# Optimization experiments

Hardware: AMD Instinct MI355X
Metric: run time of the kernel (lower is better)

The kernel has to match this reference:

```python
import jax, jax.numpy as jnp
import numpy as np

_J6 = jnp.array([[0,0,0,0,0,1],[0,0,0,0,-1,0],[0,0,0,1,0,0],[0,0,1,0,0,0],[0,-1,0,0,0,0],[1,0,0,0,0,0]], dtype=jnp.float32)
# pairs (i,j) from combinations(range(4),2)
_PI = jnp.array([0,0,0,1,1,2])
_PJ = jnp.array([1,2,3,2,3,3])

def exterior(p1, p2):
    # p1, p2: [B,T,H,4] -> Plucker line coords [B,T,H,6], L2-normalized
    L = p1[..., _PI] * p2[..., _PJ] - p1[..., _PJ] * p2[..., _PI]
    n = jnp.clip(jnp.linalg.norm(L, axis=-1, keepdims=True), 1e-12)
    return L / n

def setup_inputs() -> dict:
    key = jax.random.key(0)
    ks = jax.random.split(key, 8)
    B, T, D, H = 2, 2048, 1024, 16
    pd = 4
    s = 0.02
    return {
        "x": jax.random.normal(ks[0], (B, T, D), jnp.float32),
        "w_qkv": jax.random.normal(ks[1], (3 * D, D), jnp.float32) * s,
        "b_qkv": jnp.zeros((3 * D,), jnp.float32),
        "w1_write": jax.random.normal(ks[2], (pd * H, D), jnp.float32) * s,
        "w2_write": jax.random.normal(ks[3], (pd * H, D), jnp.float32) * s,
        "w1_read": jax.random.normal(ks[4], (pd * H, D), jnp.float32) * s,
        "w2_read": jax.random.normal(ks[5], (pd * H, D), jnp.float32) * s,
        "w_out": jax.random.normal(ks[6], (D, D), jnp.float32) * s,
        "b_out": jnp.zeros((D,), jnp.float32),
        "decay_logits": jnp.full((H,), 4.6, jnp.float32),
        "bias_scale": jnp.full((H,), 0.1, jnp.float32),
    }

def reference(x, w_qkv, b_qkv, w1_write, w2_write, w1_read, w2_read, w_out, b_out, decay_logits, bias_scale):
    B, T, D = x.shape
    H = decay_logits.shape[0]
    dh = D // H
    pd = w1_write.shape[0] // H
    scale = dh ** -0.5

    qkv = (x @ w_qkv.T + b_qkv).reshape(B, T, 3, H, dh)
    qkv = jnp.transpose(qkv, (2, 0, 3, 1, 4))  # [3,B,H,T,dh]
    q, k, v = qkv[0], qkv[1], qkv[2]
    std_logits = jnp.einsum('bhqd,bhkd->bhqk', q, k) * scale

    x_prev = jnp.concatenate([jnp.zeros((B, 1, D), x.dtype), x[:, :-1]], axis=1)
    w1 = (x_prev @ w1_write.T).reshape(B, T, H, pd)
    w2 = (x @ w2_write.T).reshape(B, T, H, pd)
    write_lines = exterior(w1, w2)  # [B,T,H,6]
    r1 = (x @ w1_read.T).reshape(B, T, H, pd)
    r2 = (x @ w2_read.T).reshape(B, T, H, pd)
    read_lines = exterior(r1, r2)

    J_write = jnp.einsum('bthi,ij->bthj', write_lines, _J6)
    incidence = jnp.einsum('bqhp,bkhp->bhqk', read_lines, J_write)  # [B,H,T,T]

    decays = jax.nn.sigmoid(decay_logits)  # [H]
    pos = jnp.arange(T, dtype=x.dtype)
    diffs = pos[:, None] - pos[None, :]  # [T,T], q - k
    past = diffs > 0
    diffs_pos = jnp.where(past, diffs, 0.0)
    weights = (decays[:, None, None] ** diffs_pos[None]) * past[None].astype(x.dtype)  # [H,T,T]

    bias = incidence * weights[None] * bias_scale[None, :, None, None]
    logits = std_logits + bias
    causal_mask = diffs < 0  # k > q -> masked
    logits = jnp.where(causal_mask[None, None], -jnp.inf, logits)
    attn = jax.nn.softmax(logits, axis=-1)
    out = jnp.einsum('bhqk,bhkd->bqhd', attn, v).reshape(B, T, D)
    return out @ w_out.T + b_out
```

## Files before the change

### kernel.cpp

```cpp
#include <hip/hip_runtime.h>
#include <hip/hip_bf16.h>

using bhalf = __hip_bfloat16;
typedef __bf16 bf16x8 __attribute__((ext_vector_type(8)));
typedef __bf16 bf16x2 __attribute__((ext_vector_type(2)));
typedef float f32x4 __attribute__((ext_vector_type(4)));

#define B_DIM 2
#define T_DIM 2048
#define D_DIM 1024
#define H_DIM 16
#define DH 64

struct bh8 { bhalf v[8]; };
struct bh4 { bhalf v[4]; };

__device__ __forceinline__ bf16x8 load_bf16x8(const bhalf* p) {
    return __builtin_bit_cast(bf16x8, *(const uint4*)p);
}
__device__ __forceinline__ bf16x8 zero_bf16x8() {
    uint4 z; z.x = 0; z.y = 0; z.z = 0; z.w = 0;
    return __builtin_bit_cast(bf16x8, z);
}
__device__ __forceinline__ void stage8_cvt(bhalf* dst, const float* src) {
    float4 a = *(const float4*)src;
    float4 b = *(const float4*)(src + 4);
    bh8 t;
    t.v[0] = __float2bfloat16(a.x); t.v[1] = __float2bfloat16(a.y);
    t.v[2] = __float2bfloat16(a.z); t.v[3] = __float2bfloat16(a.w);
    t.v[4] = __float2bfloat16(b.x); t.v[5] = __float2bfloat16(b.y);
    t.v[6] = __float2bfloat16(b.z); t.v[7] = __float2bfloat16(b.w);
    *(uint4*)dst = __builtin_bit_cast(uint4, t);
}

#define GLD16(gp, lp) __builtin_amdgcn_global_load_lds( \
    (const __attribute__((address_space(1))) void*)(gp), \
    (__attribute__((address_space(3))) void*)(lp), 16, 0, 0)

#define SX  4194304
#define SW  3145728
#define SL  65536
#define SO  1048576
__global__ __launch_bounds__(256) void cvt_all(
    const float* __restrict__ x, const float* __restrict__ wqkv,
    const float* __restrict__ w1w, const float* __restrict__ w2w,
    const float* __restrict__ w1r, const float* __restrict__ w2r,
    const float* __restrict__ wout,
    bhalf* __restrict__ xbf, bhalf* __restrict__ wcat, bhalf* __restrict__ woutbf)
{
    int i = (blockIdx.x * 256 + threadIdx.x) * 8;
    if (i < SX) { stage8_cvt(xbf + i, x + i); return; }
    i -= SX;
    if (i < SW) { stage8_cvt(wcat + i, wqkv + i); return; }
    i -= SW;
    if (i < SL) { stage8_cvt(wcat + SW + i, w1w + i); return; }
    i -= SL;
    if (i < SL) { stage8_cvt(wcat + SW + SL + i, w2w + i); return; }
    i -= SL;
    if (i < SL) { stage8_cvt(wcat + SW + 2 * SL + i, w1r + i); return; }
    i -= SL;
    if (i < SL) { stage8_cvt(wcat + SW + 3 * SL + i, w2r + i); return; }
    i -= SL;
    if (i < SO) { stage8_cvt(woutbf + i, wout + i); }
}

__device__ __forceinline__ void gemm128_mainloop(
    const bhalf* __restrict__ A, const bhalf* __restrict__ B, int K,
    bhalf* As, bhalf* Bs, f32x4 acc[4][4])
{
    const int tid = threadIdx.x;
    const int wave = tid >> 6, lane = tid & 63;
    const int ln = lane & 15, lg = lane >> 4;
    const int wr = (wave >> 1) * 64, wc = (wave & 1) * 64;
    const int lrow = lane >> 3;
    const int lcol = (lane & 7) * 8;

    for (int kt = 0; kt < K; kt += 64) {
        __syncthreads();
#pragma unroll
        for (int i = 0; i < 4; ++i) {
            int idx = __builtin_amdgcn_readfirstlane(wave * 4 + i);
            GLD16(A + (size_t)(idx * 8 + lrow) * K + kt + lcol, As + idx * 512);
            GLD16(B + (size_t)(idx * 8 + lrow) * K + kt + lcol, Bs + idx * 512);
        }
        __syncthreads();
#pragma unroll
        for (int ks = 0; ks < 2; ++ks) {
            bf16x8 af[4], bfr[4];
#pragma unroll
            for (int mt = 0; mt < 4; ++mt)
                af[mt] = load_bf16x8(As + (wr + mt * 16 + ln) * 64 + ks * 32 + lg * 8);
#pragma unroll
            for (int nt = 0; nt < 4; ++nt)
                bfr[nt] = load_bf16x8(Bs + (wc + nt * 16 + ln) * 64 + ks * 32 + lg * 8);
#pragma unroll
            for (int mt = 0; mt < 4; ++mt)
#pragma unroll
                for (int nt = 0; nt < 4; ++nt)
                    acc[mt][nt] = __builtin_amdgcn_mfma_f32_16x16x32_bf16(af[mt], bfr[nt], acc[mt][nt], 0, 0, 0);
        }
    }
}

__global__ __launch_bounds__(256) void qkv_lines_gemm128(
    const bhalf* __restrict__ x, const bhalf* __restrict__ wcat, const float* __restrict__ bqkv,
    bhalf* __restrict__ qo, bhalf* __restrict__ ko, bhalf* __restrict__ vt,
    float* __restrict__ proj)
{
    __shared__ bhalf As[128 * 64];
    __shared__ bhalf Bs[128 * 64];
    f32x4 acc[4][4] = {};
    gemm128_mainloop(x + (size_t)blockIdx.x * 128 * D_DIM,
                     wcat + (size_t)blockIdx.y * 128 * D_DIM, D_DIM, As, Bs, acc);
    const int wave = threadIdx.x >> 6, lane = threadIdx.x & 63;
    const int ln = lane & 15, lg = lane >> 4;
    const int wr = (wave >> 1) * 64, wc = (wave & 1) * 64;
    const int trip = (blockIdx.y * 128) >> 10;

    if (trip == 2) {
#pragma unroll
        for (int nt = 0; nt < 4; ++nt) {
            int n = blockIdx.y * 128 + wc + nt * 16 + ln;
            float bias = bqkv[n];
            int h = (n >> 6) & 15, d = n & 63;
#pragma unroll
            for (int mt = 0; mt < 4; ++mt) {
                int tok0 = blockIdx.x * 128 + wr + mt * 16 + lg * 4;
                int b = tok0 >> 11, t0 = tok0 & (T_DIM - 1);
                bh4 pk;
#pragma unroll
                for (int r = 0; r < 4; ++r)
                    pk.v[r] = __float2bfloat16(acc[mt][nt][r] + bias);
                *(uint2*)&vt[(((size_t)(b * H_DIM + h)) * DH + d) * T_DIM + t0] =
                    __builtin_bit_cast(uint2, pk);
            }
        }
    } else {
#pragma unroll
        for (int nt = 0; nt < 4; ++nt) {
            int n = blockIdx.y * 128 + wc + nt * 16 + ln;
            int h = (n >> 6) & 15, d = n & 63;
            float bias = (trip < 3) ? bqkv[n] : 0.f;
#pragma unroll
            for (int mt = 0; mt < 4; ++mt)
#pragma unroll
                for (int r = 0; r < 4; ++r) {
                    int tok = blockIdx.x * 128 + wr + mt * 16 + lg * 4 + r;
                    int b = tok >> 11, t = tok & (T_DIM - 1);
                    float y = acc[mt][nt][r] + bias;
                    if (trip == 0) {
                        qo[(((size_t)(b * H_DIM + h)) * T_DIM + t) * DH + d] = __float2bfloat16(y * 0.125f);
                    } else if (trip == 1) {
                        ko[(((size_t)(b * H_DIM + h)) * T_DIM + t) * DH + d] = __float2bfloat16(y);
                    } else {
                        proj[(size_t)tok * 256 + (n - 3072)] = y;
                    }
                }
        }
    }
}

__global__ __launch_bounds__(256) void out_gemm64(
    const bhalf* __restrict__ a, const bhalf* __restrict__ w, const float* __restrict__ bo,
    float* __restrict__ out)
{
    __shared__ bhalf As[64 * 64];
    __shared__ bhalf Bs[64 * 64];
    const int tid = threadIdx.x;
    const int wave = tid >> 6, lane = tid & 63;
    const int ln = lane & 15, lg = lane >> 4;
    const int lrow = lane >> 3;
    const int lcol = (lane & 7) * 8;
    const bhalf* A = a + (size_t)blockIdx.x * 64 * D_DIM;
    const bhalf* B = w + (size_t)blockIdx.y * 64 * D_DIM;
    f32x4 acc[4] = {};

    for (int kt = 0; kt < D_DIM; kt += 64) {
        __syncthreads();
#pragma unroll
        for (int i = 0; i < 2; ++i) {
            int idx = __builtin_amdgcn_readfirstlane(wave * 2 + i);
            GLD16(A + (size_t)(idx * 8 + lrow) * D_DIM + kt + lcol, As + idx * 512);
            GLD16(B + (size_t)(idx * 8 + lrow) * D_DIM + kt + lcol, Bs + idx * 512);
        }
        __syncthreads();
#pragma unroll
        for (int ks = 0; ks < 2; ++ks) {
            bf16x8 af = load_bf16x8(As + (wave * 16 + ln) * 64 + ks * 32 + lg * 8);
#pragma unroll
            for (int nt = 0; nt < 4; ++nt) {
                bf16x8 bfr = load_bf16x8(Bs + (nt * 16 + ln) * 64 + ks * 32 + lg * 8);
                acc[nt] = __builtin_amdgcn_mfma_f32_16x16x32_bf16(af, bfr, acc[nt], 0, 0, 0);
            }
        }
    }
#pragma unroll
    for (int nt = 0; nt < 4; ++nt) {
        int n = blockIdx.y * 64 + nt * 16 + ln;
        float bias = bo[n];
#pragma unroll
        for (int r = 0; r < 4; ++r) {
            int tok = blockIdx.x * 64 + wave * 16 + lg * 4 + r;
            out[(size_t)tok * D_DIM + n] = acc[nt][r] + bias;
        }
    }
}

__global__ __launch_bounds__(256) void build_lines(
    const float* __restrict__ proj, const float* __restrict__ bias_scale,
    const float* __restrict__ decay_logits,
    bhalf* __restrict__ read8, bhalf* __restrict__ jw8)
{
    int id = blockIdx.x * 256 + threadIdx.x;
    int tok = id >> 4, h = id & 15;
    int b = tok >> 11, t = tok & (T_DIM - 1);
    const float* pr = proj + (size_t)tok * 256;

    float p1[4], p2[4], r1[4], r2[4];
#pragma unroll
    for (int i = 0; i < 4; ++i) {
        p1[i] = (t > 0) ? pr[-256 + h * 4 + i] : 0.f;
        p2[i] = pr[64 + h * 4 + i];
        r1[i] = pr[128 + h * 4 + i];
        r2[i] = pr[192 + h * 4 + i];
    }
    float Lw[6], Lr[6];
    {
        Lw[0] = p1[0] * p2[1] - p1[1] * p2[0];
        Lw[1] = p1[0] * p2[2] - p1[2] * p2[0];
        Lw[2] = p1[0] * p2[3] - p1[3] * p2[0];
        Lw[3] = p1[1] * p2[2] - p1[2] * p2[1];
        Lw[4] = p1[1] * p2[3] - p1[3] * p2[1];
        Lw[5] = p1[2] * p2[3] - p1[3] * p2[2];
        float n2 = 0.f;
#pragma unroll
        for (int j = 0; j < 6; ++j) n2 += Lw[j] * Lw[j];
        float inv = 1.f / fmaxf(sqrtf(n2), 1e-12f);
#pragma unroll
        for (int j = 0; j < 6; ++j) Lw[j] *= inv;
    }
    {
        Lr[0] = r1[0] * r2[1] - r1[1] * r2[0];
        Lr[1] = r1[0] * r2[2] - r1[2] * r2[0];
        Lr[2] = r1[0] * r2[3] - r1[3] * r2[0];
        Lr[3] = r1[1] * r2[2] - r1[2] * r2[1];
        Lr[4] = r1[1] * r2[3] - r1[3] * r2[1];
        Lr[5] = r1[2] * r2[3] - r1[3] * r2[2];
        float n2 = 0.f;
#pragma unroll
        for (int j = 0; j < 6; ++j) n2 += Lr[j] * Lr[j];
        float inv = 1.f / fmaxf(sqrtf(n2), 1e-12f);
#pragma unroll
        for (int j = 0; j < 6; ++j) Lr[j] *= inv;
    }
    float decay = 1.f / (1.f + __expf(-decay_logits[h]));
    float l2d = log2f(decay);
    float bs = bias_scale[h] * exp2f(-(float)t * l2d);
    size_t base = (((size_t)(b * H_DIM + h)) * T_DIM + t) * 8;
    read8[base + 0] = __float2bfloat16(Lr[0]);
    read8[base + 1] = __float2bfloat16(Lr[1]);
    read8[base + 2] = __float2bfloat16(Lr[2]);
    read8[base + 3] = __float2bfloat16(Lr[3]);
    read8[base + 4] = __float2bfloat16(Lr[4]);
    read8[base + 5] = __float2bfloat16(Lr[5]);
    read8[base + 6] = __float2bfloat16(0.f);
    read8[base + 7] = __float2bfloat16(0.f);
    jw8[base + 0] = __float2bfloat16(Lw[5] * bs);
    jw8[base + 1] = __float2bfloat16(-Lw[4] * bs);
    jw8[base + 2] = __float2bfloat16(Lw[3] * bs);
    jw8[base + 3] = __float2bfloat16(Lw[2] * bs);
    jw8[base + 4] = __float2bfloat16(-Lw[1] * bs);
    jw8[base + 5] = __float2bfloat16(Lw[0] * bs);
    jw8[base + 6] = __float2bfloat16(0.f);
    jw8[base + 7] = __float2bfloat16(0.f);
}

template<bool DIAG>
__device__ __forceinline__ void tile_step(
    const f32x4& z0, const f32x4& z1, const f32x4& i0, const f32x4& i1,
    int rq, int kb, const float* aq, int lg, int ln, bhalf* pl, float* lp)
{
    const float LOG2E = 1.44269504f;
#pragma unroll
    for (int r = 0; r < 4; ++r) {
        float p0, p1;
        if (DIAG) {
            int diff0 = rq + lg * 4 + r - (kb + 2 * ln);
            float s0 = z0[r] + ((diff0 > 0) ? i0[r] * aq[r] : 0.f);
            p0 = (diff0 < 0) ? 0.f : exp2f(s0 * LOG2E);
            int diff1 = diff0 - 1;
            float s1 = z1[r] + ((diff1 > 0) ? i1[r] * aq[r] : 0.f);
            p1 = (diff1 < 0) ? 0.f : exp2f(s1 * LOG2E);
        } else {
            p0 = exp2f(fmaf(i0[r], aq[r], z0[r]) * LOG2E);
            p1 = exp2f(fmaf(i1[r], aq[r], z1[r]) * LOG2E);
        }
        bf16x2 h2;
        h2.x = (__bf16)p0;
        h2.y = (__bf16)p1;
        *(unsigned int*)&pl[(lg * 4 + r) * 40 + 2 * ln] = __builtin_bit_cast(unsigned int, h2);
        lp[r] += p0 + p1;
    }
}

__global__ __launch_bounds__(256) void attn_kernel(
    const bhalf* __restrict__ q, const bhalf* __restrict__ k, const bhalf* __restrict__ vt,
    const bhalf* __restrict__ read8, const bhalf* __restrict__ jw8,
    const float* __restrict__ decay_logits, bhalf* __restrict__ attn_out)
{
    __shared__ float sm[4352];
    const int wave = threadIdx.x >> 6, lane = threadIdx.x & 63;
    const int ln = lane & 15, lg = lane >> 4;
    const int bx = blockIdx.x;
    const int xcd = bx & 7;
    const int slot = bx >> 3;
    const int hbid = xcd * 4 + (slot >> 6);
    const int h = hbid & 15, b = hbid >> 4;
    const int qa = slot & 63;
    const int qb = 127 - qa;
    const int rqa = qa * 16, rqb = qb * 16;
    const size_t hb = (size_t)(b * H_DIM + h);
    const bhalf* qh = q + hb * T_DIM * DH;
    const bhalf* kh = k + hb * T_DIM * DH;
    const bhalf* vh = vt + hb * DH * T_DIM;
    const bhalf* r8 = read8 + hb * T_DIM * 8;
    const bhalf* j8 = jw8 + hb * T_DIM * 8;

    bhalf* plA = (bhalf*)sm + wave * 640;
    bhalf* plB = (bhalf*)sm + 2560 + wave * 640;

    bf16x8 zf = zero_bf16x8();
    bf16x8 qA0 = load_bf16x8(qh + (rqa + ln) * DH + lg * 8);
    bf16x8 qA1 = load_bf16x8(qh + (rqa + ln) * DH + 32 + lg * 8);
    bf16x8 qB0 = load_bf16x8(qh + (rqb + ln) * DH + lg * 8);
    bf16x8 qB1 = load_bf16x8(qh + (rqb + ln) * DH + 32 + lg * 8);
    bf16x8 rfA = (lane < 16) ? load_bf16x8(r8 + (size_t)(rqa + ln) * 8) : zf;
    bf16x8 rfB = (lane < 16) ? load_bf16x8(r8 + (size_t)(rqb + ln) * 8) : zf;

    float decay = 1.f / (1.f + __expf(-decay_logits[h]));
    float l2d = log2f(decay);
    float aqA[4], aqB[4];
#pragma unroll
    for (int r = 0; r < 4; ++r) {
        aqA[r] = exp2f((float)(rqa + lg * 4 + r) * l2d);
        aqB[r] = exp2f((float)(rqb + lg * 4 + r) * l2d);
    }

    f32x4 oA[4] = {}, oB[4] = {};
    float lpA[4] = {0.f, 0.f, 0.f, 0.f}, lpB[4] = {0.f, 0.f, 0.f, 0.f};

    const int nca = qa / 2 + 1, ncb = qb / 2 + 1;
    for (int c = wave; c < ncb; c += 4) {
        const int kb = c * 32;
        bf16x8 k00 = load_bf16x8(kh + (kb + 2 * ln) * DH + lg * 8);
        bf16x8 k01 = load_bf16x8(kh + (kb + 2 * ln) * DH + 32 + lg * 8);
        bf16x8 k10 = load_bf16x8(kh + (kb + 2 * ln + 1) * DH + lg * 8);
        bf16x8 k11 = load_bf16x8(kh + (kb + 2 * ln + 1) * DH + 32 + lg * 8);
        bf16x8 j0 = (lane < 16) ? load_bf16x8(j8 + (size_t)(kb + 2 * ln) * 8) : zf;
        bf16x8 j1 = (lane < 16) ? load_bf16x8(j8 + (size_t)(kb + 2 * ln + 1) * 8) : zf;
        bf16x8 vf0 = load_bf16x8(vh + (size_t)(ln) * T_DIM + kb + lg * 8);
        bf16x8 vf1 = load_bf16x8(vh + (size_t)(16 + ln) * T_DIM + kb + lg * 8);
        bf16x8 vf2 = load_bf16x8(vh + (size_t)(32 + ln) * T_DIM + kb + lg * 8);
        bf16x8 vf3 = load_bf16x8(vh + (size_t)(48 + ln) * T_DIM + kb + lg * 8);
        const bool doA = (c < nca);

        {
            f32x4 z0 = {}, z1 = {}, i0 = {}, i1 = {};
            z0 = __builtin_amdgcn_mfma_f32_16x16x32_bf16(qB0, k00, z0, 0, 0, 0);
            z0 = __builtin_amdgcn_mfma_f32_16x16x32_bf16(qB1, k01, z0, 0, 0, 0);
            i0 = __builtin_amdgcn_mfma_f32_16x16x32_bf16(rfB, j0, i0, 0, 0, 0);
            z1 = __builtin_amdgcn_mfma_f32_16x16x32_bf16(qB0, k10, z1, 0, 0, 0);
            z1 = __builtin_amdgcn_mfma_f32_16x16x32_bf16(qB1, k11, z1, 0, 0, 0);
            i1 = __builtin_amdgcn_mfma_f32_16x16x32_bf16(rfB, j1, i1, 0, 0, 0);
            if (c == ncb - 1) tile_step<true >(z0, z1, i0, i1, rqb, kb, aqB, lg, ln, plB, lpB);
            else              tile_step<false>(z0, z1, i0, i1, rqb, kb, aqB, lg, ln, plB, lpB);
        }
        if (doA) {
            f32x4 z0 = {}, z1 = {}, i0 = {}, i1 = {};
            z0 = __builtin_amdgcn_mfma_f32_16x16x32_bf16(qA0, k00, z0, 0, 0, 0);
            z0 = __builtin_amdgcn_mfma_f32_16x16x32_bf16(qA1, k01, z0, 0, 0, 0);
            i0 = __builtin_amdgcn_mfma_f32_16x16x32_bf16(rfA, j0, i0, 0, 0, 0);
            z1 = __builtin_amdgcn_mfma_f32_16x16x32_bf16(qA0, k10, z1, 0, 0, 0);
            z1 = __builtin_amdgcn_mfma_f32_16x16x32_bf16(qA1, k11, z1, 0, 0, 0);
            i1 = __builtin_amdgcn_mfma_f32_16x16x32_bf16(rfA, j1, i1, 0, 0, 0);
            if (c == nca - 1) tile_step<true >(z0, z1, i0, i1, rqa, kb, aqA, lg, ln, plA, lpA);
            else              tile_step<false>(z0, z1, i0, i1, rqa, kb, aqA, lg, ln, plA, lpA);
        }
        __asm__ volatile("s_waitcnt lgkmcnt(0)" ::: "memory");
        {
            bf16x8 pf = load_bf16x8(plB + ln * 40 + lg * 8);
            oB[0] = __builtin_amdgcn_mfma_f32_16x16x32_bf16(pf, vf0, oB[0], 0, 0, 0);
            oB[1] = __builtin_amdgcn_mfma_f32_16x16x32_bf16(pf, vf1, oB[1], 0, 0, 0);
            oB[2] = __builtin_amdgcn_mfma_f32_16x16x32_bf16(pf, vf2, oB[2], 0, 0, 0);
            oB[3] = __builtin_amdgcn_mfma_f32_16x16x32_bf16(pf, vf3, oB[3], 0, 0, 0);
        }
        if (doA) {
            bf16x8 pf = load_bf16x8(plA + ln * 40 + lg * 8);
            oA[0] = __builtin_amdgcn_mfma_f32_16x16x32_bf16(pf, vf0, oA[0], 0, 0, 0);
            oA[1] = __builtin_amdgcn_mfma_f32_16x16x32_bf16(pf, vf1, oA[1], 0, 0, 0);
            oA[2] = __builtin_amdgcn_mfma_f32_16x16x32_bf16(pf, vf2, oA[2], 0, 0, 0);
            oA[3] = __builtin_amdgcn_mfma_f32_16x16x32_bf16(pf, vf3, oA[3], 0, 0, 0);
        }
    }

#pragma unroll
    for (int r = 0; r < 4; ++r) {
#pragma unroll
        for (int off = 1; off < 16; off <<= 1) {
            lpA[r] += __shfl_xor(lpA[r], off, 16);
            lpB[r] += __shfl_xor(lpB[r], off, 16);
        }
    }

    const int row = threadIdx.x >> 4;
    const int c4 = (threadIdx.x & 15) * 4;

    __syncthreads();
#pragma unroll
    for (int r = 0; r < 4; ++r) {
        if (ln == 0) sm[wave * 1088 + (lg * 4 + r) * 68 + 64] = lpA[r];
#pragma unroll
        for (int nt = 0; nt < 4; ++nt)
            sm[wave * 1088 + (lg * 4 + r) * 68 + nt * 16 + ln] = oA[nt][r];
    }
    __syncthreads();
    {
        float l = 0.f;
#pragma unroll
        for (int w = 0; w < 4; ++w) l += sm[w * 1088 + row * 68 + 64];
        float4 acc = {0.f, 0.f, 0.f, 0.f};
#pragma unroll
        for (int w = 0; w < 4; ++w) {
            float4 t = *(const float4*)&sm[w * 1088 + row * 68 + c4];
            acc.x += t.x; acc.y += t.y; acc.z += t.z; acc.w += t.w;
        }
        float invl = 1.f / l;
        bh4 pk;
        pk.v[0] = __float2bfloat16(acc.x * invl);
        pk.v[1] = __float2bfloat16(acc.y * invl);
        pk.v[2] = __float2bfloat16(acc.z * invl);
        pk.v[3] = __float2bfloat16(acc.w * invl);
        size_t tok = (size_t)b * T_DIM + rqa + row;
        *(uint2*)&attn_out[tok * D_DIM + h * DH + c4] = __builtin_bit_cast(uint2, pk);
    }

    __syncthreads();
#pragma unroll
    for (int r = 0; r < 4; ++r) {
        if (ln == 0) sm[wave * 1088 + (lg * 4 + r) * 68 + 64] = lpB[r];
#pragma unroll
        for (int nt = 0; nt < 4; ++nt)
            sm[wave * 1088 + (lg * 4 + r) * 68 + nt * 16 + ln] = oB[nt][r];
    }
    __syncthreads();
    {
        float l = 0.f;
#pragma unroll
        for (int w = 0; w < 4; ++w) l += sm[w * 1088 + row * 68 + 64];
        float4 acc = {0.f, 0.f, 0.f, 0.f};
#pragma unroll
        for (int w = 0; w < 4; ++w) {
            float4 t = *(const float4*)&sm[w * 1088 + row * 68 + c4];
            acc.x += t.x; acc.y += t.y; acc.z += t.z; acc.w += t.w;
        }
        float invl = 1.f / l;
        bh4 pk;
        pk.v[0] = __float2bfloat16(acc.x * invl);
        pk.v[1] = __float2bfloat16(acc.y * invl);
        pk.v[2] = __float2bfloat16(acc.z * invl);
        pk.v[3] = __float2bfloat16(acc.w * invl);
        size_t tok = (size_t)b * T_DIM + rqb + row;
        *(uint2*)&attn_out[tok * D_DIM + h * DH + c4] = __builtin_bit_cast(uint2, pk);
    }
}

extern "C" void kernel_launch(void* const* d_in, const int* in_sizes, int n_in,
                              void* d_out, int out_size, void* d_ws, size_t ws_size,
                              hipStream_t stream)
{
    const float* x    = (const float*)d_in[0];
    const float* wqkv = (const float*)d_in[1];
    const float* bqkv = (const float*)d_in[2];
    const float* w1w  = (const float*)d_in[3];
    const float* w2w  = (const float*)d_in[4];
    const float* w1r  = (const float*)d_in[5];
    const float* w2r  = (const float*)d_in[6];
    const float* wout = (const float*)d_in[7];
    const float* bout = (const float*)d_in[8];
    const float* dlog = (const float*)d_in[9];
    const float* bsc  = (const float*)d_in[10];
    float* out = (float*)d_out;

    char* ws = (char*)d_ws;
    bhalf* qb    = (bhalf*)(ws);
    bhalf* kbuf  = (bhalf*)(ws + 8388608);
    bhalf* vtb   = (bhalf*)(ws + 16777216);
    bhalf* r8    = (bhalf*)(ws + 25165824);
    bhalf* j8    = (bhalf*)(ws + 26214400);
    float* proj  = (float*)(ws + 27262976);
    bhalf* ao    = (bhalf*)(ws + 31457280);
    bhalf* woutbf = (bhalf*)(ws + 39845888);

    bhalf* xbf  = (bhalf*)d_out;
    bhalf* wcat = (bhalf*)((char*)d_out + 8388608);

    cvt_all<<<4224, 256, 0, stream>>>(x, wqkv, w1w, w2w, w1r, w2r, wout, xbf, wcat, woutbf);
    qkv_lines_gemm128<<<dim3(32, 26), 256, 0, stream>>>(xbf, wcat, bqkv, qb, kbuf, vtb, proj);
    build_lines<<<256, 256, 0, stream>>>(proj, bsc, dlog, r8, j8);
    attn_kernel<<<2048, 256, 0, stream>>>(qb, kbuf, vtb, r8, j8, dlog, ao);
    out_gemm64<<<dim3(64, 16), 256, 0, stream>>>(ao, woutbf, bout, out);
}
```

Baseline: 283.0 us.

## Remap GEMM workgroups across XCDs, fold log2e into scales, use raw exp2

Both GEMM kernels remap the linear block id so that consecutive tiles land on the same XCD (8-way interleave), aiming for better L2 reuse of A/B tiles. The attention kernel folds log2(e) into the Q scale and the decay factors, then calls the hardware exp2 intrinsic directly, which removes a multiply and the range-checking wrapper per exponent. It also drops an explicit lgkmcnt wait before the P·V MFMAs and leaves the compiler to insert the needed waits. The raw exp2 intrinsic can lose accuracy for denormal or extreme inputs.

```diff
diff --git a/kernel.cpp b/kernel.cpp
--- a/kernel.cpp
+++ b/kernel.cpp
@@ -109,23 +109,26 @@
 {
     __shared__ bhalf As[128 * 64];
     __shared__ bhalf Bs[128 * 64];
+    const int lid = blockIdx.y * 32 + blockIdx.x;
+    const int wgid = (lid & 7) * 104 + (lid >> 3);
+    const int bx2 = wgid & 31, by2 = wgid >> 5;
     f32x4 acc[4][4] = {};
-    gemm128_mainloop(x + (size_t)blockIdx.x * 128 * D_DIM,
-                     wcat + (size_t)blockIdx.y * 128 * D_DIM, D_DIM, As, Bs, acc);
+    gemm128_mainloop(x + (size_t)bx2 * 128 * D_DIM,
+                     wcat + (size_t)by2 * 128 * D_DIM, D_DIM, As, Bs, acc);
     const int wave = threadIdx.x >> 6, lane = threadIdx.x & 63;
     const int ln = lane & 15, lg = lane >> 4;
     const int wr = (wave >> 1) * 64, wc = (wave & 1) * 64;
-    const int trip = (blockIdx.y * 128) >> 10;
+    const int trip = (by2 * 128) >> 10;
 
     if (trip == 2) {
 #pragma unroll
         for (int nt = 0; nt < 4; ++nt) {
-            int n = blockIdx.y * 128 + wc + nt * 16 + ln;
+            int n = by2 * 128 + wc + nt * 16 + ln;
             float bias = bqkv[n];
             int h = (n >> 6) & 15, d = n & 63;
 #pragma unroll
             for (int mt = 0; mt < 4; ++mt) {
-                int tok0 = blockIdx.x * 128 + wr + mt * 16 + lg * 4;
+                int tok0 = bx2 * 128 + wr + mt * 16 + lg * 4;
                 int b = tok0 >> 11, t0 = tok0 & (T_DIM - 1);
                 bh4 pk;
 #pragma unroll
@@ -138,18 +141,18 @@
     } else {
 #pragma unroll
         for (int nt = 0; nt < 4; ++nt) {
-            int n = blockIdx.y * 128 + wc + nt * 16 + ln;
+            int n = by2 * 128 + wc + nt * 16 + ln;
             int h = (n >> 6) & 15, d = n & 63;
             float bias = (trip < 3) ? bqkv[n] : 0.f;
 #pragma unroll
             for (int mt = 0; mt < 4; ++mt)
 #pragma unroll
                 for (int r = 0; r < 4; ++r) {
-                    int tok = blockIdx.x * 128 + wr + mt * 16 + lg * 4 + r;
+                    int tok = bx2 * 128 + wr + mt * 16 + lg * 4 + r;
                     int b = tok >> 11, t = tok & (T_DIM - 1);
                     float y = acc[mt][nt][r] + bias;
                     if (trip == 0) {
-                        qo[(((size_t)(b * H_DIM + h)) * T_DIM + t) * DH + d] = __float2bfloat16(y * 0.125f);
+                        qo[(((size_t)(b * H_DIM + h)) * T_DIM + t) * DH + d] = __float2bfloat16(y * 0.18033688f);
                     } else if (trip == 1) {
                         ko[(((size_t)(b * H_DIM + h)) * T_DIM + t) * DH + d] = __float2bfloat16(y);
                     } else {
@@ -166,13 +169,16 @@
 {
     __shared__ bhalf As[64 * 64];
     __shared__ bhalf Bs[64 * 64];
+    const int lid = blockIdx.y * 64 + blockIdx.x;
+    const int wgid = (lid & 7) * 128 + (lid >> 3);
+    const int bx2 = wgid & 63, by2 = wgid >> 6;
     const int tid = threadIdx.x;
     const int wave = tid >> 6, lane = tid & 63;
     const int ln = lane & 15, lg = lane >> 4;
     const int lrow = lane >> 3;
     const int lcol = (lane & 7) * 8;
-    const bhalf* A = a + (size_t)blockIdx.x * 64 * D_DIM;
-    const bhalf* B = w + (size_t)blockIdx.y * 64 * D_DIM;
+    const bhalf* A = a + (size_t)bx2 * 64 * D_DIM;
+    const bhalf* B = w + (size_t)by2 * 64 * D_DIM;
     f32x4 acc[4] = {};
 
     for (int kt = 0; kt < D_DIM; kt += 64) {
@@ -196,11 +202,11 @@
     }
 #pragma unroll
     for (int nt = 0; nt < 4; ++nt) {
-        int n = blockIdx.y * 64 + nt * 16 + ln;
+        int n = by2 * 64 + nt * 16 + ln;
         float bias = bo[n];
 #pragma unroll
         for (int r = 0; r < 4; ++r) {
-            int tok = blockIdx.x * 64 + wave * 16 + lg * 4 + r;
+            int tok = bx2 * 64 + wave * 16 + lg * 4 + r;
             out[(size_t)tok * D_DIM + n] = acc[nt][r] + bias;
         }
     }
@@ -280,20 +286,19 @@
     const f32x4& z0, const f32x4& z1, const f32x4& i0, const f32x4& i1,
     int rq, int kb, const float* aq, int lg, int ln, bhalf* pl, float* lp)
 {
-    const float LOG2E = 1.44269504f;
 #pragma unroll
     for (int r = 0; r < 4; ++r) {
         float p0, p1;
         if (DIAG) {
             int diff0 = rq + lg * 4 + r - (kb + 2 * ln);
             float s0 = z0[r] + ((diff0 > 0) ? i0[r] * aq[r] : 0.f);
-            p0 = (diff0 < 0) ? 0.f : exp2f(s0 * LOG2E);
+            p0 = (diff0 < 0) ? 0.f : __builtin_amdgcn_exp2f(s0);
             int diff1 = diff0 - 1;
             float s1 = z1[r] + ((diff1 > 0) ? i1[r] * aq[r] : 0.f);
-            p1 = (diff1 < 0) ? 0.f : exp2f(s1 * LOG2E);
+            p1 = (diff1 < 0) ? 0.f : __builtin_amdgcn_exp2f(s1);
         } else {
-            p0 = exp2f(fmaf(i0[r], aq[r], z0[r]) * LOG2E);
-            p1 = exp2f(fmaf(i1[r], aq[r], z1[r]) * LOG2E);
+            p0 = __builtin_amdgcn_exp2f(fmaf(i0[r], aq[r], z0[r]));
+            p1 = __builtin_amdgcn_exp2f(fmaf(i1[r], aq[r], z1[r]));
         }
         bf16x2 h2;
         h2.x = (__bf16)p0;
@@ -339,11 +344,12 @@
 
     float decay = 1.f / (1.f + __expf(-decay_logits[h]));
     float l2d = log2f(decay);
+    const float LOG2E = 1.44269504f;
     float aqA[4], aqB[4];
 #pragma unroll
     for (int r = 0; r < 4; ++r) {
-        aqA[r] = exp2f((float)(rqa + lg * 4 + r) * l2d);
-        aqB[r] = exp2f((float)(rqb + lg * 4 + r) * l2d);
+        aqA[r] = LOG2E * __builtin_amdgcn_exp2f((float)(rqa + lg * 4 + r) * l2d);
+        aqB[r] = LOG2E * __builtin_amdgcn_exp2f((float)(rqb + lg * 4 + r) * l2d);
     }
 
     f32x4 oA[4] = {}, oB[4] = {};
@@ -386,7 +392,6 @@
             if (c == nca - 1) tile_step<true >(z0, z1, i0, i1, rqa, kb, aqA, lg, ln, plA, lpA);
             else              tile_step<false>(z0, z1, i0, i1, rqa, kb, aqA, lg, ln, plA, lpA);
         }
-        __asm__ volatile("s_waitcnt lgkmcnt(0)" ::: "memory");
         {
             bf16x8 pf = load_bf16x8(plB + ln * 40 + lg * 8);
             oB[0] = __builtin_amdgcn_mfma_f32_16x16x32_bf16(pf, vf0, oB[0], 0, 0, 0);
```

New measurement: 288.4 us. No clear change (+1.9%).
